# Performance work log

Hardware: AMD Instinct MI355X
Metric: run time of the kernel (lower is better)

Reference implementation:

```python
import jax, jax.numpy as jnp
import numpy as np

N = 10000   # nodes
E = 160000  # edges (avg degree 16)
C = 128     # channels (multiplicity)
RB = 8      # radial basis size
HID = 64    # radial MLP hidden
AVG_NEIGH = 16.0

# e3nn-style constants: w3j(1,1,0)=delta/sqrt(3); component-normalization path alphas
C_000 = float(np.sqrt(0.5))                 # 0e x 0e -> 0e (two paths into 0e)
C_110 = float(np.sqrt(0.5) / np.sqrt(3.0))  # 1o x 1o -> 0e
C_011 = float(np.sqrt(1.5) / np.sqrt(3.0))  # 0e x 1o -> 1o (sqrt(dim=3 / 2 paths) * w3j)
C_101 = float(np.sqrt(1.5) / np.sqrt(3.0))  # 1o x 0e -> 1o


def setup_inputs() -> dict:
    key = jax.random.key(0)
    ks = jax.random.split(key, 14)
    rn = lambda k, s: jax.random.normal(k, s, dtype=jnp.float32)
    return {
        "node_attrs": rn(ks[0], (N, 10)),            # unused in forward (kept for fidelity)
        "node_feats": rn(ks[1], (N, 4 * C)),          # 128x0e (128) + 128x1o (384)
        "edge_attrs": rn(ks[2], (E, 4)),              # 1x0e + 1x1o spherical harmonics
        "edge_feats": rn(ks[3], (E, RB)),             # radial basis
        "edge_index": jax.random.randint(ks[4], (2, E), 0, N, dtype=jnp.int32),
        # linear_up (per-irrep channel mixing)
        "W_up_s": rn(ks[5], (C, C)),
        "W_up_v": rn(ks[6], (C, C)),
        # radial MLP [RB,64,64,64,weight_numel=4*C]
        "W_mlp1": rn(ks[7], (RB, HID)),
        "W_mlp2": rn(ks[8], (HID, HID)),
        "W_mlp3": rn(ks[9], (HID, HID)),
        "W_mlp4": rn(ks[10], (HID, 4 * C)),
        # output linear: 256x0e+256x1o -> 128x0e+128x1o
        "W_lin_s": rn(ks[11], (2 * C, C)),
        "W_lin_v": rn(ks[12], (2 * C, C)),
    }


def reference(node_attrs, node_feats, edge_attrs, edge_feats, edge_index,
              W_up_s, W_up_v, W_mlp1, W_mlp2, W_mlp3, W_mlp4, W_lin_s, W_lin_v):
    n = node_feats.shape[0]
    e = edge_feats.shape[0]
    sender, receiver = edge_index[0], edge_index[1]

    # split node feats into scalar (0e) and vector (1o) irreps
    s = node_feats[:, :C]                        # [N, C]
    v = node_feats[:, C:].reshape(n, C, 3)       # [N, C, 3]

    # linear_up: per-irrep channel mixing, e3nn fan-in normalization
    s = s @ (W_up_s / jnp.sqrt(jnp.float32(C)))
    v = jnp.einsum('ncm,cd->ndm', v, W_up_v / jnp.sqrt(jnp.float32(C)))

    # radial MLP -> per-edge tensor-product weights [E, 4, C]
    h = jax.nn.silu(edge_feats @ (W_mlp1 / jnp.sqrt(jnp.float32(RB))))
    h = jax.nn.silu(h @ (W_mlp2 / jnp.sqrt(jnp.float32(HID))))
    h = jax.nn.silu(h @ (W_mlp3 / jnp.sqrt(jnp.float32(HID))))
    tpw = (h @ (W_mlp4 / jnp.sqrt(jnp.float32(HID)))).reshape(e, 4, C)

    # gather sender features
    se = s[sender]                               # [E, C]
    ve = v[sender]                               # [E, C, 3]
    y0 = edge_attrs[:, :1]                       # [E, 1]
    y1 = edge_attrs[:, 1:4]                      # [E, 3]

    # uvu tensor product paths with per-edge weights
    m0a = C_000 * tpw[:, 0] * se * y0                                   # 0e x 0e -> 0e, [E,C]
    m0b = C_110 * tpw[:, 3] * jnp.einsum('ecm,em->ec', ve, y1)          # 1o x 1o -> 0e, [E,C]
    m1a = C_011 * tpw[:, 1][:, :, None] * se[:, :, None] * y1[:, None]  # 0e x 1o -> 1o, [E,C,3]
    m1b = C_101 * tpw[:, 2][:, :, None] * ve * y0[:, :, None]           # 1o x 0e -> 1o, [E,C,3]

    mji_s = jnp.concatenate([m0a, m0b], axis=1)   # [E, 2C]  (256x0e)
    mji_v = jnp.concatenate([m1a, m1b], axis=1)   # [E, 2C, 3] (256x1o)

    # scatter-sum over receiver
    msg_s = jax.ops.segment_sum(mji_s, receiver, num_segments=n)
    msg_v = jax.ops.segment_sum(mji_v, receiver, num_segments=n)

    # output linear (per-irrep) and /avg_num_neighbors
    out_s = msg_s @ (W_lin_s / jnp.sqrt(jnp.float32(2 * C)))
    out_v = jnp.einsum('ncm,cd->ndm', msg_v, W_lin_v / jnp.sqrt(jnp.float32(2 * C)))
    out = jnp.concatenate([out_s, out_v.reshape(n, 3 * C)], axis=1) / AVG_NEIGH
    return out
```

## Files before the change

kernel.cpp:

```cpp
#include <hip/hip_runtime.h>


#define N_NODES 10000
#define N_EDGES 160000

#define SVP_OFF    0u
#define MSG_OFF    2560000u
#define WP_OFF     7680000u
#define ROW_OFF    7749632u
#define ELIST_OFF  7759636u
#define SNDS_OFF   7919636u
#define EAS_OFF    8079636u
#define TPW_OFF    8719636u

#define K1_PACK    272
#define K1_HIST    313

typedef __attribute__((ext_vector_type(8))) short bf16x8;
typedef __attribute__((ext_vector_type(4))) float f32x4;

__device__ __forceinline__ float silu(float x) {
    return x / (1.0f + __expf(-x));
}
__device__ __forceinline__ short f2bf(float x) {
    unsigned u = __float_as_uint(x);
    unsigned r = (u + 0x7FFFu + ((u >> 16) & 1u)) >> 16;
    return (short)r;
}
__device__ __forceinline__ unsigned cvtpk(float lo, float hi) {
    unsigned r;
    asm("v_cvt_pk_bf16_f32 %0, %1, %2" : "=v"(r) : "v"(lo), "v"(hi));
    return r;
}
__device__ __forceinline__ float bf2f(unsigned h) {
    return __uint_as_float(h << 16);
}

constexpr float INV_SQRT_C  = 0.08838834764831845f;
constexpr float INV_SQRT_RB = 0.35355339059327373f;
constexpr float INV_SQRT_H  = 0.125f;
constexpr float OUT_SCALE   = 0.0625f * 0.0625f;
constexpr float C000 = 0.7071067811865476f;
constexpr float C110 = 0.4082482904638631f;
constexpr float C011 = 0.7071067811865476f;
constexpr float C101 = 0.7071067811865476f;

__global__ __launch_bounds__(512) void k1_pack_hist(
    const float* __restrict__ W2, const float* __restrict__ W3,
    const float* __restrict__ W4,
    const float* __restrict__ Wls, const float* __restrict__ Wlv,
    const float* __restrict__ Wus, const float* __restrict__ Wuv,
    short* __restrict__ Wp,
    const int* __restrict__ ei, int* __restrict__ cnt) {
    const int bid = blockIdx.x;
    const int tid = threadIdx.x;

    if (bid < K1_PACK) {
        int idx = bid * 512 + tid;
        if (idx < 4096) {
            int i2 = idx;
            int e = i2 & 7, l = (i2 >> 3) & 63, kt = (i2 >> 9) & 1, nt = i2 >> 10;
            int k = kt * 32 + (l >> 4) * 8 + e;
            int col = nt * 16 + (l & 15);
            Wp[idx] = f2bf(W2[k * 64 + col] * INV_SQRT_H);
        } else if (idx < 8192) {
            int i2 = idx - 4096;
            int e = i2 & 7, l = (i2 >> 3) & 63, kt = (i2 >> 9) & 1, nt = i2 >> 10;
            int k = kt * 32 + (l >> 4) * 8 + e;
            int col = nt * 16 + (l & 15);
            Wp[idx] = f2bf(W3[k * 64 + col] * INV_SQRT_H);
        } else if (idx < 40960) {
            int i2 = idx - 8192;
            int e = i2 & 7, l = (i2 >> 3) & 63, kt = (i2 >> 9) & 1, nt = i2 >> 10;
            int k = kt * 32 + (l >> 4) * 8 + e;
            int o = nt * 16 + (l & 15);
            int c = o >> 2, a = o & 3;
            Wp[idx] = f2bf(W4[k * 512 + a * 128 + c] * INV_SQRT_H);
        } else if (idx < 73728) {
            int i2 = idx - 40960;
            int e = i2 & 7, l = (i2 >> 3) & 63, kt = (i2 >> 9) & 7, nt = (i2 >> 12) & 7;
            int k = kt * 32 + (l >> 4) * 8 + e;
            int d = nt * 16 + (l & 15);
            Wp[idx] = f2bf(Wls[k * 128 + d] * OUT_SCALE);
        } else if (idx < 106496) {
            int i2 = idx - 73728;
            int e = i2 & 7, l = (i2 >> 3) & 63, kt = (i2 >> 9) & 7, nt = (i2 >> 12) & 7;
            int k = kt * 32 + (l >> 4) * 8 + e;
            int d = nt * 16 + (l & 15);
            Wp[idx] = f2bf(Wlv[k * 128 + d] * OUT_SCALE);
        } else if (idx < 122880) {
            int i2 = idx - 106496;
            int e = i2 & 7, l = (i2 >> 3) & 63, kt = (i2 >> 9) & 3, nt = (i2 >> 11) & 7;
            int k = kt * 32 + (l >> 4) * 8 + e;
            int d = nt * 16 + (l & 15);
            Wp[idx] = f2bf(Wus[k * 128 + d] * INV_SQRT_C);
        } else if (idx < 139264) {
            int i2 = idx - 122880;
            int e = i2 & 7, l = (i2 >> 3) & 63, kt = (i2 >> 9) & 3, nt = (i2 >> 11) & 7;
            int k = kt * 32 + (l >> 4) * 8 + e;
            int d = nt * 16 + (l & 15);
            Wp[idx] = f2bf(Wuv[k * 128 + d] * INV_SQRT_C);
        }
        return;
    }
    int e = (bid - K1_PACK) * 512 + tid;
    if (e < N_EDGES) atomicAdd(&cnt[ei[N_EDGES + e]], 1);
}

__global__ __launch_bounds__(512) void k2_scan_nodeup(
    const int*   __restrict__ cnt,
    int*         __restrict__ row,
    int*         __restrict__ cursor,
    const float* __restrict__ nf,
    const short* __restrict__ Wp,
    uint2*       __restrict__ svp) {
    __shared__ __align__(8) short stage[16 * 128 * 4];
    const int bid = blockIdx.x;
    const int tid = threadIdx.x;

    if (bid == 0) {
        int* part = (int*)stage;
        const int t = tid;
        const int base = t * 20;
        int s = 0;
        #pragma unroll
        for (int i = 0; i < 20; ++i) {
            int idx = base + i;
            s += (idx < N_NODES) ? cnt[idx] : 0;
        }
        part[t] = s;
        __syncthreads();
        for (int off = 1; off < 512; off <<= 1) {
            int v = (t >= off) ? part[t - off] : 0;
            __syncthreads();
            part[t] += v;
            __syncthreads();
        }
        int run = part[t] - s;
        #pragma unroll
        for (int i = 0; i < 20; ++i) {
            int idx = base + i;
            if (idx < N_NODES) {
                row[idx] = run;
                cursor[idx] = run;
                run += cnt[idx];
            }
        }
        if (t == 511) row[N_NODES] = part[511];
        return;
    }

    const short* Wusp = Wp + 106496;
    const short* Wuvp = Wp + 122880;
    const int l   = tid & 63;
    const int w   = tid >> 6;
    const int sec = w & 3;
    const int nth = w >> 2;
    const int r16 = l & 15;
    const int g4  = l >> 4;
    const int n0  = (bid - 1) * 16;
    const float* nfrow = nf + (size_t)(n0 + r16) * 512;

    bf16x8 a[4];
    if (sec == 0) {
        #pragma unroll
        for (int kt = 0; kt < 4; ++kt) {
            const float* p = nfrow + kt * 32 + g4 * 8;
            float4 x0 = *(const float4*)p;
            float4 x1 = *(const float4*)(p + 4);
            bf16x8 t;
            t[0] = f2bf(x0.x); t[1] = f2bf(x0.y); t[2] = f2bf(x0.z); t[3] = f2bf(x0.w);
            t[4] = f2bf(x1.x); t[5] = f2bf(x1.y); t[6] = f2bf(x1.z); t[7] = f2bf(x1.w);
            a[kt] = t;
        }
    } else {
        const int m = sec - 1;
        #pragma unroll
        for (int kt = 0; kt < 4; ++kt) {
            const float* p = nfrow + 128 + 3 * (kt * 32 + g4 * 8) + m;
            bf16x8 t;
            #pragma unroll
            for (int e = 0; e < 8; ++e) t[e] = f2bf(p[3 * e]);
            a[kt] = t;
        }
    }
    const short* Wq = (sec == 0) ? Wusp : Wuvp;
    #pragma unroll
    for (int ni = 0; ni < 4; ++ni) {
        const int nt = nth * 4 + ni;
        f32x4 c = {0.f, 0.f, 0.f, 0.f};
        #pragma unroll
        for (int kt = 0; kt < 4; ++kt) {
            bf16x8 b = *(const bf16x8*)(Wq + ((nt * 4 + kt) * 64 + l) * 8);
            c = __builtin_amdgcn_mfma_f32_16x16x32_bf16(a[kt], b, c, 0, 0, 0);
        }
        const int d = nt * 16 + r16;
        #pragma unroll
        for (int r = 0; r < 4; ++r) {
            const int nl = g4 * 4 + r;
            stage[(nl * 128 + d) * 4 + sec] = f2bf(c[r]);
        }
    }
    __syncthreads();
    const uint2* st = (const uint2*)stage;
    uint2* outp = svp + (size_t)n0 * 128;
    #pragma unroll
    for (int j = 0; j < 4; ++j) {
        const int idx = tid + 512 * j;
        outp[idx] = st[idx];
    }
}

__global__ void k_scatter(const int* __restrict__ ei, int* __restrict__ cursor,
                          const float* __restrict__ edge_attrs,
                          int* __restrict__ elist, int* __restrict__ snds,
                          float4* __restrict__ eas) {
    int e = blockIdx.x * 256 + threadIdx.x;
    if (e < N_EDGES) {
        int snd = ei[e];
        int r = ei[N_EDGES + e];
        int pos = atomicAdd(&cursor[r], 1);
        elist[pos] = e;
        snds[pos] = snd;
        eas[pos] = ((const float4*)edge_attrs)[e];
    }
}

__global__ __launch_bounds__(256) void k_edge(
    const float* __restrict__ edge_feats,
    const float* __restrict__ W1,
    const short* __restrict__ Wp,
    unsigned short* __restrict__ tpw16) {
    __shared__ __align__(16) short h0[64][72];
    __shared__ __align__(16) short h1[64][72];
    __shared__ __align__(16) uint2 stg[4][16][17];

    const short* W2p = Wp;
    const short* W3p = Wp + 4096;
    const short* W4p = Wp + 8192;
    const int tid = threadIdx.x;
    const int l   = tid & 63;
    const int w   = tid >> 6;
    const int r16 = l & 15;
    const int g4  = l >> 4;
    const int base = blockIdx.x * 64;
    const int erow = w * 16 + r16;

    {
        const size_t p = (size_t)(base + erow);
        float4 f0 = ((const float4*)edge_feats)[p * 2 + 0];
        float4 f1 = ((const float4*)edge_feats)[p * 2 + 1];
        float ef[8] = {f0.x, f0.y, f0.z, f0.w, f1.x, f1.y, f1.z, f1.w};
        const int j0 = g4 * 16;
        float acc[16];
        #pragma unroll
        for (int jj = 0; jj < 16; ++jj) acc[jj] = 0.f;
        #pragma unroll
        for (int k = 0; k < 8; ++k) {
            const float* wr = W1 + k * 64 + j0;
            float4 w0 = *(const float4*)(wr + 0);
            float4 w1 = *(const float4*)(wr + 4);
            float4 w2 = *(const float4*)(wr + 8);
            float4 w3 = *(const float4*)(wr + 12);
            const float hk = ef[k];
            acc[0]  = fmaf(hk, w0.x, acc[0]);  acc[1]  = fmaf(hk, w0.y, acc[1]);
            acc[2]  = fmaf(hk, w0.z, acc[2]);  acc[3]  = fmaf(hk, w0.w, acc[3]);
            acc[4]  = fmaf(hk, w1.x, acc[4]);  acc[5]  = fmaf(hk, w1.y, acc[5]);
            acc[6]  = fmaf(hk, w1.z, acc[6]);  acc[7]  = fmaf(hk, w1.w, acc[7]);
            acc[8]  = fmaf(hk, w2.x, acc[8]);  acc[9]  = fmaf(hk, w2.y, acc[9]);
            acc[10] = fmaf(hk, w2.z, acc[10]); acc[11] = fmaf(hk, w2.w, acc[11]);
            acc[12] = fmaf(hk, w3.x, acc[12]); acc[13] = fmaf(hk, w3.y, acc[13]);
            acc[14] = fmaf(hk, w3.z, acc[14]); acc[15] = fmaf(hk, w3.w, acc[15]);
        }
        unsigned pk[8];
        #pragma unroll
        for (int q = 0; q < 8; ++q)
            pk[q] = cvtpk(silu(acc[2*q] * INV_SQRT_RB),
                          silu(acc[2*q + 1] * INV_SQRT_RB));
        uint4 A; A.x = pk[0]; A.y = pk[1]; A.z = pk[2]; A.w = pk[3];
        uint4 B; B.x = pk[4]; B.y = pk[5]; B.z = pk[6]; B.w = pk[7];
        *(uint4*)&h0[erow][j0]     = A;
        *(uint4*)&h0[erow][j0 + 8] = B;
    }

    {
        bf16x8 a0 = *(const bf16x8*)&h0[erow][g4 * 8];
        bf16x8 a1 = *(const bf16x8*)&h0[erow][32 + g4 * 8];
        #pragma unroll
        for (int nt = 0; nt < 4; ++nt) {
            bf16x8 b0 = *(const bf16x8*)(W2p + ((nt * 2 + 0) * 64 + l) * 8);
            bf16x8 b1 = *(const bf16x8*)(W2p + ((nt * 2 + 1) * 64 + l) * 8);
            f32x4 c = {0.f, 0.f, 0.f, 0.f};
            c = __builtin_amdgcn_mfma_f32_16x16x32_bf16(a0, b0, c, 0, 0, 0);
            c = __builtin_amdgcn_mfma_f32_16x16x32_bf16(a1, b1, c, 0, 0, 0);
            unsigned u01 = cvtpk(silu(c[0]), silu(c[1]));
            unsigned u23 = cvtpk(silu(c[2]), silu(c[3]));
            h1[w * 16 + g4 * 4 + 0][nt * 16 + r16] = (short)(u01 & 0xffffu);
            h1[w * 16 + g4 * 4 + 1][nt * 16 + r16] = (short)(u01 >> 16);
            h1[w * 16 + g4 * 4 + 2][nt * 16 + r16] = (short)(u23 & 0xffffu);
            h1[w * 16 + g4 * 4 + 3][nt * 16 + r16] = (short)(u23 >> 16);
        }
    }

    {
        bf16x8 a0 = *(const bf16x8*)&h1[erow][g4 * 8];
        bf16x8 a1 = *(const bf16x8*)&h1[erow][32 + g4 * 8];
        #pragma unroll
        for (int nt = 0; nt < 4; ++nt) {
            bf16x8 b0 = *(const bf16x8*)(W3p + ((nt * 2 + 0) * 64 + l) * 8);
            bf16x8 b1 = *(const bf16x8*)(W3p + ((nt * 2 + 1) * 64 + l) * 8);
            f32x4 c = {0.f, 0.f, 0.f, 0.f};
            c = __builtin_amdgcn_mfma_f32_16x16x32_bf16(a0, b0, c, 0, 0, 0);
            c = __builtin_amdgcn_mfma_f32_16x16x32_bf16(a1, b1, c, 0, 0, 0);
            unsigned u01 = cvtpk(silu(c[0]), silu(c[1]));
            unsigned u23 = cvtpk(silu(c[2]), silu(c[3]));
            h0[w * 16 + g4 * 4 + 0][nt * 16 + r16] = (short)(u01 & 0xffffu);
            h0[w * 16 + g4 * 4 + 1][nt * 16 + r16] = (short)(u01 >> 16);
            h0[w * 16 + g4 * 4 + 2][nt * 16 + r16] = (short)(u23 & 0xffffu);
            h0[w * 16 + g4 * 4 + 3][nt * 16 + r16] = (short)(u23 >> 16);
        }
    }

    {
        bf16x8 ha0 = *(const bf16x8*)&h0[erow][g4 * 8];
        bf16x8 ha1 = *(const bf16x8*)&h0[erow][32 + g4 * 8];
        const int ebase = base + w * 16;
        const int er = (l >> 3) & 7;
        const int ck = l & 7;
        unsigned short* twb0 = tpw16 + (size_t)(ebase + er) * 512 + ck * 8;
        unsigned short* twb1 = tpw16 + (size_t)(ebase + er + 8) * 512 + ck * 8;
        uint2 (*sw)[17] = stg[w];

        #pragma unroll 2
        for (int grp = 0; grp < 8; ++grp) {
            #pragma unroll
            for (int h = 0; h < 4; ++h) {
                const int nt = grp * 4 + h;
                bf16x8 w0 = *(const bf16x8*)(W4p + ((nt * 2 + 0) * 64 + l) * 8);
                bf16x8 w1 = *(const bf16x8*)(W4p + ((nt * 2 + 1) * 64 + l) * 8);
                f32x4 c = {0.f, 0.f, 0.f, 0.f};
                c = __builtin_amdgcn_mfma_f32_16x16x32_bf16(w0, ha0, c, 0, 0, 0);
                c = __builtin_amdgcn_mfma_f32_16x16x32_bf16(w1, ha1, c, 0, 0, 0);
                uint2 u;
                u.x = cvtpk(c[0], c[1]);
                u.y = cvtpk(c[2], c[3]);
                sw[r16][h * 4 + g4] = u;
            }
            uint2 a0 = sw[er][ck * 2];
            uint2 a1 = sw[er][ck * 2 + 1];
            uint2 b0 = sw[er + 8][ck * 2];
            uint2 b1 = sw[er + 8][ck * 2 + 1];
            {
                uint4 v; v.x = a0.x; v.y = a0.y; v.z = a1.x; v.w = a1.y;
                *(uint4*)(twb0 + grp * 64) = v;
            }
            {
                uint4 v; v.x = b0.x; v.y = b0.y; v.z = b1.x; v.w = b1.y;
                *(uint4*)(twb1 + grp * 64) = v;
            }
        }
    }
}

__global__ __launch_bounds__(128) void k_gather(
    const int*    __restrict__ row,
    const int*    __restrict__ elist,
    const int*    __restrict__ snds,
    const float4* __restrict__ eas,
    const unsigned short* __restrict__ tpw16,
    const uint2*  __restrict__ svp,
    unsigned short* __restrict__ msg16) {
    const int nidx = blockIdx.x;
    const int c = threadIdx.x;
    const int beg = row[nidx];
    const int end = row[nidx + 1];

    float a0 = 0.f, a1 = 0.f, a2 = 0.f, a3 = 0.f,
          a4 = 0.f, a5 = 0.f, a6 = 0.f, a7 = 0.f;

    #pragma unroll 4
    for (int i = beg; i < end; ++i) {
        const int e   = elist[i];
        const int snd = snds[i];
        const float4 ea = eas[i];
        const float y0 = ea.x, y10 = ea.y, y11 = ea.z, y12 = ea.w;

        const uint2 u  = *(const uint2*)(tpw16 + (size_t)e * 512 + c * 4);
        const uint2 sv = svp[(size_t)snd * 128 + c];
        const float t0 = bf2f(u.x & 0xffffu);
        const float t1 = bf2f(u.x >> 16);
        const float t2 = bf2f(u.y & 0xffffu);
        const float t3 = bf2f(u.y >> 16);
        const float se  = bf2f(sv.x & 0xffffu);
        const float ve0 = bf2f(sv.x >> 16);
        const float ve1 = bf2f(sv.y & 0xffffu);
        const float ve2 = bf2f(sv.y >> 16);

        a0 = fmaf(C000 * t0 * y0, se, a0);
        const float dvy = ve0 * y10 + ve1 * y11 + ve2 * y12;
        a1 = fmaf(C110 * t3, dvy, a1);
        const float c011t = C011 * t1 * se;
        a2 = fmaf(c011t, y10, a2);
        a3 = fmaf(c011t, y11, a3);
        a4 = fmaf(c011t, y12, a4);
        const float c101t = C101 * t2 * y0;
        a5 = fmaf(c101t, ve0, a5);
        a6 = fmaf(c101t, ve1, a6);
        a7 = fmaf(c101t, ve2, a7);
    }

    unsigned short* m = msg16 + (size_t)nidx * 1024;
    m[c]       = (unsigned short)f2bf(a0);
    m[128 + c] = (unsigned short)f2bf(a1);
    m[256 + c] = (unsigned short)f2bf(a2);
    m[512 + c] = (unsigned short)f2bf(a3);
    m[768 + c] = (unsigned short)f2bf(a4);
    m[384 + c] = (unsigned short)f2bf(a5);
    m[640 + c] = (unsigned short)f2bf(a6);
    m[896 + c] = (unsigned short)f2bf(a7);
}

__global__ __launch_bounds__(512) void k_node_out(
    const unsigned short* __restrict__ msg16,
    const short* __restrict__ Wlsp,
    const short* __restrict__ Wlvp,
    float*       __restrict__ out) {
    const int tid = threadIdx.x;
    const int l   = tid & 63;
    const int w   = tid >> 6;
    const int sec = w & 3;
    const int nth = w >> 2;
    const int r16 = l & 15;
    const int g4  = l >> 4;
    const int n0  = blockIdx.x * 16;
    const unsigned short* mrow = msg16 + (size_t)(n0 + r16) * 1024 + sec * 256;

    bf16x8 a[8];
    #pragma unroll
    for (int kt = 0; kt < 8; ++kt)
        a[kt] = *(const bf16x8*)(mrow + kt * 32 + g4 * 8);

    const short* Wq = (sec == 0) ? Wlsp : Wlvp;
    #pragma unroll
    for (int ni = 0; ni < 4; ++ni) {
        const int nt = nth * 4 + ni;
        f32x4 c = {0.f, 0.f, 0.f, 0.f};
        #pragma unroll
        for (int kt = 0; kt < 8; ++kt) {
            bf16x8 b = *(const bf16x8*)(Wq + ((nt * 8 + kt) * 64 + l) * 8);
            c = __builtin_amdgcn_mfma_f32_16x16x32_bf16(a[kt], b, c, 0, 0, 0);
        }
        const int d = nt * 16 + r16;
        #pragma unroll
        for (int r = 0; r < 4; ++r) {
            const size_t n = n0 + g4 * 4 + r;
            if (sec == 0) out[n * 512 + d] = c[r];
            else          out[n * 512 + 128 + 3 * d + (sec - 1)] = c[r];
        }
    }
}

extern "C" void kernel_launch(void* const* d_in, const int* in_sizes, int n_in,
                              void* d_out, int out_size, void* d_ws, size_t ws_size,
                              hipStream_t stream) {
    const float* node_feats = (const float*)d_in[1];
    const float* edge_attrs = (const float*)d_in[2];
    const float* edge_feats = (const float*)d_in[3];
    const int*   edge_index = (const int*)d_in[4];
    const float* W_up_s = (const float*)d_in[5];
    const float* W_up_v = (const float*)d_in[6];
    const float* W_mlp1 = (const float*)d_in[7];
    const float* W_mlp2 = (const float*)d_in[8];
    const float* W_mlp3 = (const float*)d_in[9];
    const float* W_mlp4 = (const float*)d_in[10];
    const float* W_lin_s = (const float*)d_in[11];
    const float* W_lin_v = (const float*)d_in[12];

    float* ws     = (float*)d_ws;
    uint2* svp    = (uint2*)(ws + SVP_OFF);
    unsigned short* msg16 = (unsigned short*)(ws + MSG_OFF);
    short* Wp     = (short*)(ws + WP_OFF);
    short* Wlsp   = Wp + 40960;
    short* Wlvp   = Wp + 73728;
    int*   row    = (int*)(ws + ROW_OFF);
    int*   elist  = (int*)(ws + ELIST_OFF);
    int*   snds   = (int*)(ws + SNDS_OFF);
    float4* eas   = (float4*)(ws + EAS_OFF);
    unsigned short* tpw16 = (unsigned short*)(ws + TPW_OFF);
    int*   cnt    = (int*)msg16;
    int*   cursor = cnt + N_NODES;
    float* out_f  = (float*)d_out;

    (void)hipMemsetAsync(cnt, 0, 2 * N_NODES * sizeof(int), stream);
    k1_pack_hist<<<K1_PACK + K1_HIST, 512, 0, stream>>>(
        W_mlp2, W_mlp3, W_mlp4, W_lin_s, W_lin_v, W_up_s, W_up_v, Wp,
        edge_index, cnt);
    k2_scan_nodeup<<<1 + 625, 512, 0, stream>>>(
        cnt, row, cursor, node_feats, Wp, svp);
    k_scatter<<<(N_EDGES + 255) / 256, 256, 0, stream>>>(
        edge_index, cursor, edge_attrs, elist, snds, eas);
    k_edge<<<N_EDGES / 64, 256, 0, stream>>>(edge_feats, W_mlp1, Wp, tpw16);
    k_gather<<<N_NODES, 128, 0, stream>>>(row, elist, snds, eas, tpw16, svp, msg16);
    k_node_out<<<625, 512, 0, stream>>>(msg16, Wlsp, Wlvp, out_f);
}
```

Baseline: 198.9 us.

## Compute edge MLP in receiver-sorted order so gather reads tpw contiguously

```diff
diff --git a/kernel.cpp b/kernel.cpp
--- a/kernel.cpp
+++ b/kernel.cpp
@@ -11,7 +11,8 @@
 #define ELIST_OFF  7759636u
 #define SNDS_OFF   7919636u
 #define EAS_OFF    8079636u
-#define TPW_OFF    8719636u
+#define EFS_OFF    8719636u
+#define TPW_OFF    9999636u
 
 #define K1_PACK    272
 #define K1_HIST    313
@@ -213,31 +214,33 @@
 
 __global__ void k_scatter(const int* __restrict__ ei, int* __restrict__ cursor,
                           const float* __restrict__ edge_attrs,
-                          int* __restrict__ elist, int* __restrict__ snds,
-                          float4* __restrict__ eas) {
+                          const float* __restrict__ edge_feats,
+                          int* __restrict__ snds,
+                          float4* __restrict__ eas, float4* __restrict__ efs) {
     int e = blockIdx.x * 256 + threadIdx.x;
     if (e < N_EDGES) {
         int snd = ei[e];
         int r = ei[N_EDGES + e];
         int pos = atomicAdd(&cursor[r], 1);
-        elist[pos] = e;
         snds[pos] = snd;
         eas[pos] = ((const float4*)edge_attrs)[e];
-    }
-}
-
-__global__ __launch_bounds__(256) void k_edge(
-    const float* __restrict__ edge_feats,
+        efs[(size_t)pos * 2 + 0] = ((const float4*)edge_feats)[(size_t)e * 2 + 0];
+        efs[(size_t)pos * 2 + 1] = ((const float4*)edge_feats)[(size_t)e * 2 + 1];
+    }
+}
+
+__global__ __launch_bounds__(256) void k_edge_mfma(
+    const float4* __restrict__ efs,
     const float* __restrict__ W1,
-    const short* __restrict__ Wp,
+    const short* __restrict__ W2p,
+    const short* __restrict__ W3p,
+    const short* __restrict__ W4p,
+    int ne,
     unsigned short* __restrict__ tpw16) {
     __shared__ __align__(16) short h0[64][72];
     __shared__ __align__(16) short h1[64][72];
     __shared__ __align__(16) uint2 stg[4][16][17];
 
-    const short* W2p = Wp;
-    const short* W3p = Wp + 4096;
-    const short* W4p = Wp + 8192;
     const int tid = threadIdx.x;
     const int l   = tid & 63;
     const int w   = tid >> 6;
@@ -247,9 +250,10 @@
     const int erow = w * 16 + r16;
 
     {
-        const size_t p = (size_t)(base + erow);
-        float4 f0 = ((const float4*)edge_feats)[p * 2 + 0];
-        float4 f1 = ((const float4*)edge_feats)[p * 2 + 1];
+        const int pos = base + erow;
+        const size_t p = (size_t)((pos < ne) ? pos : 0);
+        float4 f0 = efs[p * 2 + 0];
+        float4 f1 = efs[p * 2 + 1];
         float ef[8] = {f0.x, f0.y, f0.z, f0.w, f1.x, f1.y, f1.z, f1.w};
         const int j0 = g4 * 16;
         float acc[16];
@@ -327,6 +331,8 @@
         const int ebase = base + w * 16;
         const int er = (l >> 3) & 7;
         const int ck = l & 7;
+        const bool v0 = (ebase + er) < ne;
+        const bool v1 = (ebase + er + 8) < ne;
         unsigned short* twb0 = tpw16 + (size_t)(ebase + er) * 512 + ck * 8;
         unsigned short* twb1 = tpw16 + (size_t)(ebase + er + 8) * 512 + ck * 8;
         uint2 (*sw)[17] = stg[w];
@@ -350,11 +356,11 @@
             uint2 a1 = sw[er][ck * 2 + 1];
             uint2 b0 = sw[er + 8][ck * 2];
             uint2 b1 = sw[er + 8][ck * 2 + 1];
-            {
+            if (v0) {
                 uint4 v; v.x = a0.x; v.y = a0.y; v.z = a1.x; v.w = a1.y;
                 *(uint4*)(twb0 + grp * 64) = v;
             }
-            {
+            if (v1) {
                 uint4 v; v.x = b0.x; v.y = b0.y; v.z = b1.x; v.w = b1.y;
                 *(uint4*)(twb1 + grp * 64) = v;
             }
@@ -364,7 +370,6 @@
 
 __global__ __launch_bounds__(128) void k_gather(
     const int*    __restrict__ row,
-    const int*    __restrict__ elist,
     const int*    __restrict__ snds,
     const float4* __restrict__ eas,
     const unsigned short* __restrict__ tpw16,
@@ -380,12 +385,11 @@
 
     #pragma unroll 4
     for (int i = beg; i < end; ++i) {
-        const int e   = elist[i];
         const int snd = snds[i];
         const float4 ea = eas[i];
         const float y0 = ea.x, y10 = ea.y, y11 = ea.z, y12 = ea.w;
 
-        const uint2 u  = *(const uint2*)(tpw16 + (size_t)e * 512 + c * 4);
+        const uint2 u  = *(const uint2*)(tpw16 + (size_t)i * 512 + c * 4);
         const uint2 sv = svp[(size_t)snd * 128 + c];
         const float t0 = bf2f(u.x & 0xffffu);
         const float t1 = bf2f(u.x >> 16);
@@ -480,12 +484,15 @@
     uint2* svp    = (uint2*)(ws + SVP_OFF);
     unsigned short* msg16 = (unsigned short*)(ws + MSG_OFF);
     short* Wp     = (short*)(ws + WP_OFF);
+    short* W2p    = Wp;
+    short* W3p    = Wp + 4096;
+    short* W4p    = Wp + 8192;
     short* Wlsp   = Wp + 40960;
     short* Wlvp   = Wp + 73728;
     int*   row    = (int*)(ws + ROW_OFF);
-    int*   elist  = (int*)(ws + ELIST_OFF);
     int*   snds   = (int*)(ws + SNDS_OFF);
     float4* eas   = (float4*)(ws + EAS_OFF);
+    float4* efs   = (float4*)(ws + EFS_OFF);
     unsigned short* tpw16 = (unsigned short*)(ws + TPW_OFF);
     int*   cnt    = (int*)msg16;
     int*   cursor = cnt + N_NODES;
@@ -498,8 +505,9 @@
     k2_scan_nodeup<<<1 + 625, 512, 0, stream>>>(
         cnt, row, cursor, node_feats, Wp, svp);
     k_scatter<<<(N_EDGES + 255) / 256, 256, 0, stream>>>(
-        edge_index, cursor, edge_attrs, elist, snds, eas);
-    k_edge<<<N_EDGES / 64, 256, 0, stream>>>(edge_feats, W_mlp1, Wp, tpw16);
-    k_gather<<<N_NODES, 128, 0, stream>>>(row, elist, snds, eas, tpw16, svp, msg16);
+        edge_index, cursor, edge_attrs, edge_feats, snds, eas, efs);
+    k_edge_mfma<<<(N_EDGES + 63) / 64, 256, 0, stream>>>(
+        efs, W_mlp1, W2p, W3p, W4p, N_EDGES, tpw16);
+    k_gather<<<N_NODES, 128, 0, stream>>>(row, snds, eas, tpw16, svp, msg16);
     k_node_out<<<625, 512, 0, stream>>>(msg16, Wlsp, Wlvp, out_f);
 }
```

After: 187.9 us. -5.6%, faster.
